# Kernel tuning notes

Hardware: AMD Instinct MI355X
Metric: run time of the kernel (lower is better)

## Reference

```python
import jax, jax.numpy as jnp
import numpy as np

B, S, D = 2, 2048, 1024
H = 16
HD = D // H  # 64

def setup_inputs() -> dict:
    key = jax.random.key(0)
    ks = jax.random.split(key, 5)
    scale = 0.02
    x = jax.random.normal(ks[0], (B, S, D), dtype=jnp.float32)
    w_attn = jax.random.normal(ks[1], (D, 3 * D), dtype=jnp.float32) * scale
    b_attn = jnp.zeros((3 * D,), dtype=jnp.float32)
    w_proj = jax.random.normal(ks[2], (D, D), dtype=jnp.float32) * scale
    b_proj = jnp.zeros((D,), dtype=jnp.float32)
    return {"x": x, "w_attn": w_attn, "b_attn": b_attn, "w_proj": w_proj, "b_proj": b_proj}

def reference(x, w_attn, b_attn, w_proj, b_proj):
    b, s, d = x.shape
    qkv = x @ w_attn + b_attn                      # [B,S,3D]
    q, k, v = jnp.split(qkv, 3, axis=-1)
    # [B,H,S,HD]
    q = q.reshape(b, s, H, HD).transpose(0, 2, 1, 3)
    k = k.reshape(b, s, H, HD).transpose(0, 2, 1, 3)
    v = v.reshape(b, s, H, HD).transpose(0, 2, 1, 3)
    scores = jnp.einsum('bhqd,bhkd->bhqk', q, k) * (1.0 / np.sqrt(HD))
    causal = jnp.tril(jnp.ones((s, s), dtype=bool))
    scores = jnp.where(causal[None, None], scores, -jnp.inf)
    attn = jax.nn.softmax(scores, axis=-1)
    out = jnp.einsum('bhqk,bhkd->bhqd', attn, v)   # [B,H,S,HD]
    out = out.transpose(0, 2, 1, 3).reshape(b, s, d)
    return out @ w_proj + b_proj
```

## Files before the change

kernel.cpp:

```cpp
#include <hip/hip_runtime.h>

#define B_  2
#define S_  2048
#define D_  1024
#define H_  16
#define HD_ 64
#define TD_ 3072
#define M_  (B_*S_)
#define NWORK_ 24

using bf16x8 = __attribute__((ext_vector_type(8))) short;
using bf16x4 = __attribute__((ext_vector_type(4))) short;
using f32x4  = __attribute__((ext_vector_type(4))) float;

typedef __attribute__((address_space(1))) unsigned int uint_g;
typedef __attribute__((address_space(3))) unsigned int uint_l;

#define MFMA32 __builtin_amdgcn_mfma_f32_16x16x32_bf16

#if defined(__has_builtin)
#if __has_builtin(__builtin_amdgcn_mfma_f32_16x16x16_bf16_1k)
#define MFMA16(a,b,c) __builtin_amdgcn_mfma_f32_16x16x16_bf16_1k(a,b,c,0,0,0)
#define HAVE_MFMA16 1
#elif __has_builtin(__builtin_amdgcn_mfma_f32_16x16x16bf16_1k)
#define MFMA16(a,b,c) __builtin_amdgcn_mfma_f32_16x16x16bf16_1k(a,b,c,0,0,0)
#define HAVE_MFMA16 1
#endif
#endif
#ifndef HAVE_MFMA16
static __device__ __forceinline__ f32x4 MFMA16_stub(bf16x4 a, bf16x4 b, f32x4 c) { return c; }
#define MFMA16(a,b,c) MFMA16_stub(a,b,c)
#endif

static __device__ __forceinline__ short f2bf(float f) {
    unsigned u = __float_as_uint(f);
    u += 0x7FFFu + ((u >> 16) & 1u);
    return (short)(u >> 16);
}
static __device__ __forceinline__ unsigned pack2bf(float a, float b) {
    return (unsigned)(unsigned short)f2bf(a) | ((unsigned)(unsigned short)f2bf(b) << 16);
}
static __device__ __forceinline__ void gload_lds16(const short* g, short* l) {
    __builtin_amdgcn_global_load_lds((const uint_g*)g, (uint_l*)l, 16, 0, 0);
}
static __device__ __forceinline__ void unpack8(uint4 u, float* f) {
    unsigned a0 = u.x, a1 = u.y, a2 = u.z, a3 = u.w;
    f[0] = __uint_as_float(a0 << 16); f[1] = __uint_as_float(a0 & 0xFFFF0000u);
    f[2] = __uint_as_float(a1 << 16); f[3] = __uint_as_float(a1 & 0xFFFF0000u);
    f[4] = __uint_as_float(a2 << 16); f[5] = __uint_as_float(a2 & 0xFFFF0000u);
    f[6] = __uint_as_float(a3 << 16); f[7] = __uint_as_float(a3 & 0xFFFF0000u);
}

__global__ void cast_x_kernel(const float* __restrict__ x, short* __restrict__ xb, int n4) {
    int i = blockIdx.x * blockDim.x + threadIdx.x;
    if (i >= n4) return;
    float4 v = *((const float4*)x + i);
    short4 o;
    o.x = f2bf(v.x); o.y = f2bf(v.y); o.z = f2bf(v.z); o.w = f2bf(v.w);
    *((short4*)xb + i) = o;
}

__global__ __launch_bounds__(256)
void wtrans_kernel(const float* __restrict__ W, short* __restrict__ Wt, int K, int N) {
    __shared__ float T[32][33];
    int n0 = blockIdx.x * 32, k0 = blockIdx.y * 32;
    int tx = threadIdx.x & 31, ty = threadIdx.x >> 5;
    #pragma unroll
    for (int i = 0; i < 4; ++i)
        T[ty + i * 8][tx] = W[(size_t)(k0 + ty + i * 8) * N + n0 + tx];
    __syncthreads();
    #pragma unroll
    for (int i = 0; i < 4; ++i)
        Wt[(size_t)(n0 + ty + i * 8) * K + k0 + tx] = f2bf(T[tx][ty + i * 8]);
}

__global__ __launch_bounds__(256)
void vtrans_kernel(const short* __restrict__ V, short* __restrict__ Vt) {
    __shared__ short T[32][33];
    int p  = blockIdx.z;
    int s0 = blockIdx.x * 32;
    int d0 = blockIdx.y * 32;
    int tx = threadIdx.x & 31, ty = threadIdx.x >> 5;
    const short* Vp  = V  + (size_t)p * S_ * HD_;
    short*       Vtp = Vt + (size_t)p * HD_ * S_;
    #pragma unroll
    for (int i = 0; i < 4; ++i)
        T[ty + i * 8][tx] = Vp[(s0 + ty + i * 8) * HD_ + d0 + tx];
    __syncthreads();
    #pragma unroll
    for (int i = 0; i < 4; ++i)
        Vtp[(size_t)(d0 + ty + i * 8) * S_ + s0 + tx] = T[tx][ty + i * 8];
}

template<int MODE>
__global__ __launch_bounds__(256)
void gemm_mfma_kernel(const short* __restrict__ A, const short* __restrict__ Bt,
                      const float* __restrict__ bias, float* __restrict__ Cf,
                      short* __restrict__ Qo, short* __restrict__ Ko, short* __restrict__ Vo,
                      int M, int N, int K) {
    __shared__ __align__(16) short As[128 * 32];
    __shared__ __align__(16) short Bs[128 * 32];

    const int tid  = threadIdx.x;
    const int w    = tid >> 6, lane = tid & 63;
    const int quad = lane >> 4, l16 = lane & 15;
    const int wr = (w >> 1) * 64, wc = (w & 1) * 64;
    const int rowBase = blockIdx.y * 128, colBase = blockIdx.x * 128;

    f32x4 acc[4][4];
    const f32x4 zero = {0.f, 0.f, 0.f, 0.f};
    #pragma unroll
    for (int i = 0; i < 4; ++i)
        #pragma unroll
        for (int j = 0; j < 4; ++j) acc[i][j] = zero;

    const int srow = lane >> 2;
    const int scol = (lane & 3) * 8;

    for (int k0 = 0; k0 < K; k0 += 32) {
        __syncthreads();
        gload_lds16(A  + (size_t)(rowBase + w * 16 + srow)      * K + k0 + scol, &As[(w * 16) * 32]);
        gload_lds16(A  + (size_t)(rowBase + 64 + w * 16 + srow) * K + k0 + scol, &As[(64 + w * 16) * 32]);
        gload_lds16(Bt + (size_t)(colBase + w * 16 + srow)      * K + k0 + scol, &Bs[(w * 16) * 32]);
        gload_lds16(Bt + (size_t)(colBase + 64 + w * 16 + srow) * K + k0 + scol, &Bs[(64 + w * 16) * 32]);
        __syncthreads();

        bf16x8 af[4], bf[4];
        #pragma unroll
        for (int t = 0; t < 4; ++t) {
            af[t] = *(const bf16x8*)&As[(wr + t * 16 + l16) * 32 + quad * 8];
            bf[t] = *(const bf16x8*)&Bs[(wc + t * 16 + l16) * 32 + quad * 8];
        }
        #pragma unroll
        for (int i = 0; i < 4; ++i)
            #pragma unroll
            for (int j = 0; j < 4; ++j)
                acc[i][j] = MFMA32(af[i], bf[j], acc[i][j], 0, 0, 0);
    }

    if (MODE == 0) {
        #pragma unroll
        for (int i = 0; i < 4; ++i) {
            int row = rowBase + wr + i * 16 + quad * 4;
            #pragma unroll
            for (int j = 0; j < 4; ++j) {
                int col = colBase + wc + j * 16 + l16;
                float bv = bias[col];
                #pragma unroll
                for (int r = 0; r < 4; ++r)
                    Cf[(size_t)(row + r) * N + col] = acc[i][j][r] + bv;
            }
        }
    } else {
        #pragma unroll
        for (int j = 0; j < 4; ++j) {
            int col = colBase + wc + j * 16 + l16;
            int sel = col >> 10, cr = col & 1023;
            int h = cr >> 6, d = cr & 63;
            float bv  = bias[col];
            short* dst = (sel == 0) ? Qo : (sel == 1) ? Ko : Vo;
            float  scl = (sel == 0) ? 0.125f : 1.0f;
            #pragma unroll
            for (int i = 0; i < 4; ++i) {
                int row = rowBase + wr + i * 16 + quad * 4;
                #pragma unroll
                for (int r = 0; r < 4; ++r) {
                    int rw = row + r;
                    int bb = rw >> 11, s = rw & 2047;
                    dst[((size_t)(bb * H_ + h) * S_ + s) * HD_ + d] =
                        f2bf((acc[i][j][r] + bv) * scl);
                }
            }
        }
    }
}

__global__ __launch_bounds__(256, 3)
void flash_mfma_kernel(const short* __restrict__ Qg, const short* __restrict__ Kg,
                       const short* __restrict__ Vtg,
                       short* __restrict__ pO, float* __restrict__ pl) {
    __shared__ __align__(16) short Ks[64][72];
    __shared__ __align__(16) short Vs[64][72];

    const int plane_id = blockIdx.x;
    const int y = blockIdx.y;
    int qi, kc;
    if (y < 8) { qi = y; kc = 0; }
    else       { qi = 8 + ((y - 8) >> 1); kc = (y - 8) & 1; }
    int nkt = 2 * qi + 2 - kc * 16;
    if (nkt > 16) nkt = 16;
    const int kvOrigin = kc * 1024;

    const int tid  = threadIdx.x;
    const int w    = tid >> 6, lane = tid & 63;
    const int quad = lane >> 4, l16 = lane & 15;
    const int qBase = qi * 128;
    const size_t plane = (size_t)plane_id * S_ * HD_;

    const int sr0 = tid >> 3;
    const int sc0 = (tid & 7) * 8;

    const int qsubA = qBase + w * 32;
    const short* QrowA = Qg + plane + (size_t)(qsubA + l16) * HD_ + quad * 8;
    const bf16x8 qa0 = *(const bf16x8*)(QrowA);
    const bf16x8 qa1 = *(const bf16x8*)(QrowA + 32);
    const short* QrowB = QrowA + 16 * HD_;
    const bf16x8 qb0 = *(const bf16x8*)(QrowB);
    const bf16x8 qb1 = *(const bf16x8*)(QrowB + 32);

    f32x4 oA[4], oB[4];
    const f32x4 zero = {0.f, 0.f, 0.f, 0.f};
    #pragma unroll
    for (int i = 0; i < 4; ++i) { oA[i] = zero; oB[i] = zero; }
    float lA = 0.f, lB = 0.f;
    const int q_globA = qsubA + l16;
    const int q_globB = qsubA + 16 + l16;
    const int q_wave_max = qsubA + 31;

    uint4 ka0, ka1, va0, va1;
    ka0 = *(const uint4*)(Kg  + plane + (size_t)(kvOrigin + sr0)      * HD_ + sc0);
    ka1 = *(const uint4*)(Kg  + plane + (size_t)(kvOrigin + sr0 + 32) * HD_ + sc0);
    va0 = *(const uint4*)(Vtg + plane + (size_t)sr0        * S_ + kvOrigin + sc0);
    va1 = *(const uint4*)(Vtg + plane + (size_t)(sr0 + 32) * S_ + kvOrigin + sc0);

    for (int j = 0; j < nkt; ++j) {
        __syncthreads();
        *(uint4*)&Ks[sr0][sc0]      = ka0;
        *(uint4*)&Ks[sr0 + 32][sc0] = ka1;
        *(uint4*)&Vs[sr0][sc0]      = va0;
        *(uint4*)&Vs[sr0 + 32][sc0] = va1;
        __syncthreads();

        if (j + 1 < nkt) {
            const int kvB = kvOrigin + (j + 1) * 64;
            ka0 = *(const uint4*)(Kg  + plane + (size_t)(kvB + sr0)      * HD_ + sc0);
            ka1 = *(const uint4*)(Kg  + plane + (size_t)(kvB + sr0 + 32) * HD_ + sc0);
            va0 = *(const uint4*)(Vtg + plane + (size_t)sr0        * S_ + kvB + sc0);
            va1 = *(const uint4*)(Vtg + plane + (size_t)(sr0 + 32) * S_ + kvB + sc0);
        }

        const int kvBase = kvOrigin + j * 64;
        if (kvBase > q_wave_max) continue;

        f32x4 sA[4], sB[4];
        #pragma unroll
        for (int ct = 0; ct < 4; ++ct) {
            bf16x8 kf0 = *(const bf16x8*)&Ks[ct * 16 + l16][quad * 8];
            bf16x8 kf1 = *(const bf16x8*)&Ks[ct * 16 + l16][32 + quad * 8];
            f32x4 a = zero, b = zero;
            a = MFMA32(kf0, qa0, a, 0, 0, 0);
            a = MFMA32(kf1, qa1, a, 0, 0, 0);
            b = MFMA32(kf0, qb0, b, 0, 0, 0);
            b = MFMA32(kf1, qb1, b, 0, 0, 0);
            sA[ct] = a; sB[ct] = b;
        }

        if (kvBase + 63 > qsubA) {
            #pragma unroll
            for (int ct = 0; ct < 4; ++ct) {
                int kv = kvBase + ct * 16 + quad * 4;
                #pragma unroll
                for (int r = 0; r < 4; ++r)
                    if (kv + r > q_globA) sA[ct][r] = -3.0e38f;
            }
        }
        if (kvBase + 63 > qsubA + 16) {
            #pragma unroll
            for (int ct = 0; ct < 4; ++ct) {
                int kv = kvBase + ct * 16 + quad * 4;
                #pragma unroll
                for (int r = 0; r < 4; ++r)
                    if (kv + r > q_globB) sB[ct][r] = -3.0e38f;
            }
        }

        #pragma unroll
        for (int ct = 0; ct < 4; ++ct) {
            float pa0 = __expf(sA[ct][0]), pa1 = __expf(sA[ct][1]);
            float pa2 = __expf(sA[ct][2]), pa3 = __expf(sA[ct][3]);
            float pb0 = __expf(sB[ct][0]), pb1 = __expf(sB[ct][1]);
            float pb2 = __expf(sB[ct][2]), pb3 = __expf(sB[ct][3]);
            lA += (pa0 + pa1) + (pa2 + pa3);
            lB += (pb0 + pb1) + (pb2 + pb3);
            bf16x4 pA, pB;
            *(unsigned*)&pA       = pack2bf(pa0, pa1);
            *((unsigned*)&pA + 1) = pack2bf(pa2, pa3);
            *(unsigned*)&pB       = pack2bf(pb0, pb1);
            *((unsigned*)&pB + 1) = pack2bf(pb2, pb3);
            #pragma unroll
            for (int dt = 0; dt < 4; ++dt) {
                bf16x4 vfr = *(const bf16x4*)&Vs[dt * 16 + l16][ct * 16 + quad * 4];
                oA[dt] = MFMA16(vfr, pA, oA[dt]);
                oB[dt] = MFMA16(vfr, pB, oB[dt]);
            }
        }
    }

    lA += __shfl_xor(lA, 16); lA += __shfl_xor(lA, 32);
    lB += __shfl_xor(lB, 16); lB += __shfl_xor(lB, 32);
    const size_t lbase = ((size_t)plane_id * NWORK_ + y) * 128 + w * 32;
    if (quad == 0) {
        pl[lbase + l16]      = lA;
        pl[lbase + 16 + l16] = lB;
    }

    __syncthreads();
    short* Pw = (w < 2) ? &Ks[w * 32][0] : &Vs[(w - 2) * 32][0];
    #pragma unroll
    for (int dt = 0; dt < 4; ++dt) {
        uint2 ua, ub;
        ua.x = pack2bf(oA[dt][0], oA[dt][1]);
        ua.y = pack2bf(oA[dt][2], oA[dt][3]);
        ub.x = pack2bf(oB[dt][0], oB[dt][1]);
        ub.y = pack2bf(oB[dt][2], oB[dt][3]);
        *(uint2*)&Pw[l16 * 72 + dt * 16 + quad * 4]        = ua;
        *(uint2*)&Pw[(16 + l16) * 72 + dt * 16 + quad * 4] = ub;
    }
    __builtin_amdgcn_s_waitcnt(0xC07F);
    short* outBase = pO + (((size_t)plane_id * NWORK_ + y) * 128 + w * 32) * 64;
    #pragma unroll
    for (int pass = 0; pass < 4; ++pass) {
        int r  = pass * 8 + (lane >> 3);
        int cs = (lane & 7) * 8;
        uint4 vv = *(const uint4*)&Pw[r * 72 + cs];
        *(uint4*)(outBase + r * 64 + cs) = vv;
    }
}

__global__ __launch_bounds__(256)
void reduce_kernel(const short* __restrict__ pO, const float* __restrict__ pl,
                   short* __restrict__ atb) {
    const int plane_id = blockIdx.x, qi = blockIdx.y;
    const int h = plane_id & (H_ - 1), b = plane_id >> 4;
    const int tid = threadIdx.x;
    const int row = tid >> 1;
    const int cb  = (tid & 1) * 32;

    int t0, nch;
    if (qi < 8) { t0 = qi; nch = 1; }
    else        { t0 = 8 + 2 * (qi - 8); nch = 2; }

    const size_t pbase = (((size_t)plane_id * NWORK_ + t0) * 128 + row) * 64 + cb;
    float f[32], g[8];
    unpack8(*(const uint4*)(pO + pbase),      f);
    unpack8(*(const uint4*)(pO + pbase + 8),  f + 8);
    unpack8(*(const uint4*)(pO + pbase + 16), f + 16);
    unpack8(*(const uint4*)(pO + pbase + 24), f + 24);
    float l = pl[((size_t)plane_id * NWORK_ + t0) * 128 + row];
    if (nch == 2) {
        #pragma unroll
        for (int c = 0; c < 4; ++c) {
            unpack8(*(const uint4*)(pO + pbase + 8192 + c * 8), g);
            #pragma unroll
            for (int i = 0; i < 8; ++i) f[c * 8 + i] += g[i];
        }
        l += pl[((size_t)plane_id * NWORK_ + t0 + 1) * 128 + row];
    }
    const float inv = 1.0f / l;
    short* dst = atb + (size_t)(b * S_ + qi * 128 + row) * D_ + h * HD_ + cb;
    #pragma unroll
    for (int c = 0; c < 4; ++c) {
        uint2 o2;
        o2.x = pack2bf(f[c * 8 + 0] * inv, f[c * 8 + 1] * inv);
        o2.y = pack2bf(f[c * 8 + 2] * inv, f[c * 8 + 3] * inv);
        uint2 o3;
        o3.x = pack2bf(f[c * 8 + 4] * inv, f[c * 8 + 5] * inv);
        o3.y = pack2bf(f[c * 8 + 6] * inv, f[c * 8 + 7] * inv);
        uint4 ov; ov.x = o2.x; ov.y = o2.y; ov.z = o3.x; ov.w = o3.y;
        *(uint4*)(dst + c * 8) = ov;
    }
}

extern "C" void kernel_launch(void* const* d_in, const int* in_sizes, int n_in,
                              void* d_out, int out_size, void* d_ws, size_t ws_size,
                              hipStream_t stream) {
    const float* x      = (const float*)d_in[0];
    const float* w_attn = (const float*)d_in[1];
    const float* b_attn = (const float*)d_in[2];
    const float* w_proj = (const float*)d_in[3];
    const float* b_proj = (const float*)d_in[4];
    float* out = (float*)d_out;

    char* ws = (char*)d_ws;
    short* xb  = (short*)ws; ws += (size_t)M_ * D_ * 2;
    short* wat = (short*)ws; ws += (size_t)TD_ * D_ * 2;
    short* wpt = (short*)ws; ws += (size_t)D_ * D_ * 2;
    short* qg  = (short*)ws; ws += (size_t)M_ * D_ * 2;
    short* kg  = (short*)ws; ws += (size_t)M_ * D_ * 2;
    short* vg  = (short*)ws; ws += (size_t)M_ * D_ * 2;
    short* vtg = (short*)ws; ws += (size_t)M_ * D_ * 2;
    short* atb = (short*)ws; ws += (size_t)M_ * D_ * 2;

    short* pO = (short*)d_ws;
    float* pl = (float*)((char*)d_ws + (size_t)32 * NWORK_ * 128 * 64 * 2);

    cast_x_kernel<<<(M_ * D_ / 4 + 255) / 256, 256, 0, stream>>>(x, xb, M_ * D_ / 4);
    wtrans_kernel<<<dim3(TD_ / 32, D_ / 32), 256, 0, stream>>>(w_attn, wat, D_, TD_);
    wtrans_kernel<<<dim3(D_ / 32, D_ / 32), 256, 0, stream>>>(w_proj, wpt, D_, D_);

    gemm_mfma_kernel<1><<<dim3(TD_ / 128, M_ / 128), 256, 0, stream>>>(
        xb, wat, b_attn, nullptr, qg, kg, vg, M_, TD_, D_);

    vtrans_kernel<<<dim3(S_ / 32, HD_ / 32, B_ * H_), 256, 0, stream>>>(vg, vtg);

    flash_mfma_kernel<<<dim3(B_ * H_, NWORK_), 256, 0, stream>>>(qg, kg, vtg, pO, pl);

    reduce_kernel<<<dim3(B_ * H_, S_ / 128), 256, 0, stream>>>(pO, pl, atb);

    gemm_mfma_kernel<0><<<dim3(D_ / 128, M_ / 128), 256, 0, stream>>>(
        atb, wpt, b_proj, out, nullptr, nullptr, nullptr, M_, D_, D_);
}
```

Before: 200.5 us.

## Split flash work finer, fuse prep kernels, shrink output GEMM tile

```diff
diff --git a/kernel.cpp b/kernel.cpp
--- a/kernel.cpp
+++ b/kernel.cpp
@@ -7,7 +7,8 @@
 #define HD_ 64
 #define TD_ 3072
 #define M_  (B_*S_)
-#define NWORK_ 24
+#define NWORK_ 40
+#define PO_SPLIT_ 896
 
 using bf16x8 = __attribute__((ext_vector_type(8))) short;
 using bf16x4 = __attribute__((ext_vector_type(4))) short;
@@ -50,21 +51,37 @@
     f[4] = __uint_as_float(a2 << 16); f[5] = __uint_as_float(a2 & 0xFFFF0000u);
     f[6] = __uint_as_float(a3 << 16); f[7] = __uint_as_float(a3 & 0xFFFF0000u);
 }
-
-__global__ void cast_x_kernel(const float* __restrict__ x, short* __restrict__ xb, int n4) {
-    int i = blockIdx.x * blockDim.x + threadIdx.x;
-    if (i >= n4) return;
-    float4 v = *((const float4*)x + i);
-    short4 o;
-    o.x = f2bf(v.x); o.y = f2bf(v.y); o.z = f2bf(v.z); o.w = f2bf(v.w);
-    *((short4*)xb + i) = o;
+static __device__ __forceinline__ const short* pO_ptr_c(const short* A, const short* B, int item) {
+    return (item < PO_SPLIT_) ? A + (size_t)item * 8192 : B + (size_t)(item - PO_SPLIT_) * 8192;
+}
+static __device__ __forceinline__ short* pO_ptr(short* A, short* B, int item) {
+    return (item < PO_SPLIT_) ? A + (size_t)item * 8192 : B + (size_t)(item - PO_SPLIT_) * 8192;
 }
 
 __global__ __launch_bounds__(256)
-void wtrans_kernel(const float* __restrict__ W, short* __restrict__ Wt, int K, int N) {
+void prep_kernel(const float* __restrict__ x, short* __restrict__ xb,
+                 const float* __restrict__ w_attn, short* __restrict__ wat,
+                 const float* __restrict__ w_proj, short* __restrict__ wpt) {
     __shared__ float T[32][33];
-    int n0 = blockIdx.x * 32, k0 = blockIdx.y * 32;
-    int tx = threadIdx.x & 31, ty = threadIdx.x >> 5;
+    const int id  = blockIdx.x;
+    const int tid = threadIdx.x;
+    if (id < 4096) {
+        int i = id * 256 + tid;
+        float4 v = *((const float4*)x + i);
+        short4 o;
+        o.x = f2bf(v.x); o.y = f2bf(v.y); o.z = f2bf(v.z); o.w = f2bf(v.w);
+        *((short4*)xb + i) = o;
+        return;
+    }
+    const float* W; short* Wt; int K, N, n0, k0;
+    if (id < 7168) {
+        int i = id - 4096; W = w_attn; Wt = wat; K = D_; N = TD_;
+        n0 = (i % 96) * 32; k0 = (i / 96) * 32;
+    } else {
+        int i = id - 7168; W = w_proj; Wt = wpt; K = D_; N = D_;
+        n0 = (i & 31) * 32; k0 = (i >> 5) * 32;
+    }
+    int tx = tid & 31, ty = tid >> 5;
     #pragma unroll
     for (int i = 0; i < 4; ++i)
         T[ty + i * 8][tx] = W[(size_t)(k0 + ty + i * 8) * N + n0 + tx];
@@ -92,12 +109,10 @@
         Vtp[(size_t)(d0 + ty + i * 8) * S_ + s0 + tx] = T[tx][ty + i * 8];
 }
 
-template<int MODE>
 __global__ __launch_bounds__(256)
-void gemm_mfma_kernel(const short* __restrict__ A, const short* __restrict__ Bt,
-                      const float* __restrict__ bias, float* __restrict__ Cf,
-                      short* __restrict__ Qo, short* __restrict__ Ko, short* __restrict__ Vo,
-                      int M, int N, int K) {
+void qkv_gemm_kernel(const short* __restrict__ A, const short* __restrict__ Bt,
+                     const float* __restrict__ bias,
+                     short* __restrict__ Qo, short* __restrict__ Ko, short* __restrict__ Vo) {
     __shared__ __align__(16) short As[128 * 32];
     __shared__ __align__(16) short Bs[128 * 32];
 
@@ -106,6 +121,7 @@
     const int quad = lane >> 4, l16 = lane & 15;
     const int wr = (w >> 1) * 64, wc = (w & 1) * 64;
     const int rowBase = blockIdx.y * 128, colBase = blockIdx.x * 128;
+    const int K = D_;
 
     f32x4 acc[4][4];
     const f32x4 zero = {0.f, 0.f, 0.f, 0.f};
@@ -138,58 +154,46 @@
                 acc[i][j] = MFMA32(af[i], bf[j], acc[i][j], 0, 0, 0);
     }
 
-    if (MODE == 0) {
+    #pragma unroll
+    for (int j = 0; j < 4; ++j) {
+        int col = colBase + wc + j * 16 + l16;
+        int sel = col >> 10, cr = col & 1023;
+        int h = cr >> 6, d = cr & 63;
+        float bv  = bias[col];
+        short* dst = (sel == 0) ? Qo : (sel == 1) ? Ko : Vo;
+        float  scl = (sel == 0) ? 0.125f : 1.0f;
         #pragma unroll
         for (int i = 0; i < 4; ++i) {
             int row = rowBase + wr + i * 16 + quad * 4;
             #pragma unroll
-            for (int j = 0; j < 4; ++j) {
-                int col = colBase + wc + j * 16 + l16;
-                float bv = bias[col];
-                #pragma unroll
-                for (int r = 0; r < 4; ++r)
-                    Cf[(size_t)(row + r) * N + col] = acc[i][j][r] + bv;
+            for (int r = 0; r < 4; ++r) {
+                int rw = row + r;
+                int bb = rw >> 11, s = rw & 2047;
+                dst[((size_t)(bb * H_ + h) * S_ + s) * HD_ + d] =
+                    f2bf((acc[i][j][r] + bv) * scl);
             }
         }
-    } else {
-        #pragma unroll
-        for (int j = 0; j < 4; ++j) {
-            int col = colBase + wc + j * 16 + l16;
-            int sel = col >> 10, cr = col & 1023;
-            int h = cr >> 6, d = cr & 63;
-            float bv  = bias[col];
-            short* dst = (sel == 0) ? Qo : (sel == 1) ? Ko : Vo;
-            float  scl = (sel == 0) ? 0.125f : 1.0f;
-            #pragma unroll
-            for (int i = 0; i < 4; ++i) {
-                int row = rowBase + wr + i * 16 + quad * 4;
-                #pragma unroll
-                for (int r = 0; r < 4; ++r) {
-                    int rw = row + r;
-                    int bb = rw >> 11, s = rw & 2047;
-                    dst[((size_t)(bb * H_ + h) * S_ + s) * HD_ + d] =
-                        f2bf((acc[i][j][r] + bv) * scl);
-                }
-            }
-        }
-    }
-}
-
-__global__ __launch_bounds__(256, 3)
+    }
+}
+
+__global__ __launch_bounds__(256, 6)
 void flash_mfma_kernel(const short* __restrict__ Qg, const short* __restrict__ Kg,
                        const short* __restrict__ Vtg,
-                       short* __restrict__ pO, float* __restrict__ pl) {
+                       short* __restrict__ poA, short* __restrict__ poB,
+                       float* __restrict__ pl) {
     __shared__ __align__(16) short Ks[64][72];
     __shared__ __align__(16) short Vs[64][72];
 
     const int plane_id = blockIdx.x;
-    const int y = blockIdx.y;
-    int qi, kc;
-    if (y < 8) { qi = y; kc = 0; }
-    else       { qi = 8 + ((y - 8) >> 1); kc = (y - 8) & 1; }
-    int nkt = 2 * qi + 2 - kc * 16;
-    if (nkt > 16) nkt = 16;
-    const int kvOrigin = kc * 1024;
+    const int y = (int)(gridDim.y - 1) - (int)blockIdx.y;
+    const int g = (y < 4) ? 0 : (y < 12) ? 1 : (y < 24) ? 2 : 3;
+    const int rem = y - 2 * g * (g + 1);
+    const int qi = 4 * g + rem / (g + 1);
+    const int kc = rem - (rem / (g + 1)) * (g + 1);
+    int nkt = 2 * qi + 2 - kc * 8;
+    if (nkt > 8) nkt = 8;
+    const int kvOrigin = kc * 512;
+    const int item = plane_id * NWORK_ + y;
 
     const int tid  = threadIdx.x;
     const int w    = tid >> 6, lane = tid & 63;
@@ -298,7 +302,7 @@
 
     lA += __shfl_xor(lA, 16); lA += __shfl_xor(lA, 32);
     lB += __shfl_xor(lB, 16); lB += __shfl_xor(lB, 32);
-    const size_t lbase = ((size_t)plane_id * NWORK_ + y) * 128 + w * 32;
+    const size_t lbase = (size_t)item * 128 + w * 32;
     if (quad == 0) {
         pl[lbase + l16]      = lA;
         pl[lbase + 16 + l16] = lB;
@@ -317,7 +321,7 @@
         *(uint2*)&Pw[(16 + l16) * 72 + dt * 16 + quad * 4] = ub;
     }
     __builtin_amdgcn_s_waitcnt(0xC07F);
-    short* outBase = pO + (((size_t)plane_id * NWORK_ + y) * 128 + w * 32) * 64;
+    short* outBase = pO_ptr(poA, poB, item) + (size_t)(w * 32) * 64;
     #pragma unroll
     for (int pass = 0; pass < 4; ++pass) {
         int r  = pass * 8 + (lane >> 3);
@@ -328,46 +332,99 @@
 }
 
 __global__ __launch_bounds__(256)
-void reduce_kernel(const short* __restrict__ pO, const float* __restrict__ pl,
-                   short* __restrict__ atb) {
+void reduce_kernel(const short* __restrict__ poA, const short* __restrict__ poB,
+                   const float* __restrict__ pl, short* __restrict__ atb) {
     const int plane_id = blockIdx.x, qi = blockIdx.y;
     const int h = plane_id & (H_ - 1), b = plane_id >> 4;
     const int tid = threadIdx.x;
     const int row = tid >> 1;
     const int cb  = (tid & 1) * 32;
 
-    int t0, nch;
-    if (qi < 8) { t0 = qi; nch = 1; }
-    else        { t0 = 8 + 2 * (qi - 8); nch = 2; }
-
-    const size_t pbase = (((size_t)plane_id * NWORK_ + t0) * 128 + row) * 64 + cb;
-    float f[32], g[8];
-    unpack8(*(const uint4*)(pO + pbase),      f);
-    unpack8(*(const uint4*)(pO + pbase + 8),  f + 8);
-    unpack8(*(const uint4*)(pO + pbase + 16), f + 16);
-    unpack8(*(const uint4*)(pO + pbase + 24), f + 24);
-    float l = pl[((size_t)plane_id * NWORK_ + t0) * 128 + row];
-    if (nch == 2) {
+    const int g = qi >> 2;
+    const int t0 = 2 * g * (g + 1) + (qi - 4 * g) * (g + 1);
+    const int nch = g + 1;
+    const int item0 = plane_id * NWORK_ + t0;
+
+    float f[32];
+    #pragma unroll
+    for (int i = 0; i < 32; ++i) f[i] = 0.f;
+    float l = 0.f;
+    for (int ch = 0; ch < nch; ++ch) {
+        const short* p = pO_ptr_c(poA, poB, item0 + ch) + (size_t)row * 64 + cb;
+        float g8[8];
         #pragma unroll
         for (int c = 0; c < 4; ++c) {
-            unpack8(*(const uint4*)(pO + pbase + 8192 + c * 8), g);
-            #pragma unroll
-            for (int i = 0; i < 8; ++i) f[c * 8 + i] += g[i];
-        }
-        l += pl[((size_t)plane_id * NWORK_ + t0 + 1) * 128 + row];
+            unpack8(*(const uint4*)(p + c * 8), g8);
+            #pragma unroll
+            for (int i = 0; i < 8; ++i) f[c * 8 + i] += g8[i];
+        }
+        l += pl[(size_t)(item0 + ch) * 128 + row];
     }
     const float inv = 1.0f / l;
     short* dst = atb + (size_t)(b * S_ + qi * 128 + row) * D_ + h * HD_ + cb;
     #pragma unroll
     for (int c = 0; c < 4; ++c) {
-        uint2 o2;
-        o2.x = pack2bf(f[c * 8 + 0] * inv, f[c * 8 + 1] * inv);
-        o2.y = pack2bf(f[c * 8 + 2] * inv, f[c * 8 + 3] * inv);
-        uint2 o3;
-        o3.x = pack2bf(f[c * 8 + 4] * inv, f[c * 8 + 5] * inv);
-        o3.y = pack2bf(f[c * 8 + 6] * inv, f[c * 8 + 7] * inv);
-        uint4 ov; ov.x = o2.x; ov.y = o2.y; ov.z = o3.x; ov.w = o3.y;
+        uint4 ov;
+        ov.x = pack2bf(f[c * 8 + 0] * inv, f[c * 8 + 1] * inv);
+        ov.y = pack2bf(f[c * 8 + 2] * inv, f[c * 8 + 3] * inv);
+        ov.z = pack2bf(f[c * 8 + 4] * inv, f[c * 8 + 5] * inv);
+        ov.w = pack2bf(f[c * 8 + 6] * inv, f[c * 8 + 7] * inv);
         *(uint4*)(dst + c * 8) = ov;
+    }
+}
+
+__global__ __launch_bounds__(256)
+void gemm2_mfma_kernel(const short* __restrict__ A, const short* __restrict__ Bt,
+                       const float* __restrict__ bias, float* __restrict__ Cf) {
+    __shared__ __align__(16) short As[64 * 32];
+    __shared__ __align__(16) short Bs[128 * 32];
+
+    const int tid  = threadIdx.x;
+    const int w    = tid >> 6, lane = tid & 63;
+    const int quad = lane >> 4, l16 = lane & 15;
+    const int rowBase = blockIdx.y * 64, colBase = blockIdx.x * 128;
+    const int K = D_;
+
+    f32x4 acc[4][2];
+    const f32x4 zero = {0.f, 0.f, 0.f, 0.f};
+    #pragma unroll
+    for (int i = 0; i < 4; ++i) { acc[i][0] = zero; acc[i][1] = zero; }
+
+    const int srow = lane >> 2;
+    const int scol = (lane & 3) * 8;
+
+    for (int k0 = 0; k0 < K; k0 += 32) {
+        __syncthreads();
+        gload_lds16(A  + (size_t)(rowBase + w * 16 + srow)      * K + k0 + scol, &As[(w * 16) * 32]);
+        gload_lds16(Bt + (size_t)(colBase + w * 16 + srow)      * K + k0 + scol, &Bs[(w * 16) * 32]);
+        gload_lds16(Bt + (size_t)(colBase + 64 + w * 16 + srow) * K + k0 + scol, &Bs[(64 + w * 16) * 32]);
+        __syncthreads();
+
+        bf16x8 af[4], bf[2];
+        #pragma unroll
+        for (int t = 0; t < 4; ++t)
+            af[t] = *(const bf16x8*)&As[(t * 16 + l16) * 32 + quad * 8];
+        #pragma unroll
+        for (int t = 0; t < 2; ++t)
+            bf[t] = *(const bf16x8*)&Bs[(w * 32 + t * 16 + l16) * 32 + quad * 8];
+        #pragma unroll
+        for (int i = 0; i < 4; ++i)
+            #pragma unroll
+            for (int j = 0; j < 2; ++j)
+                acc[i][j] = MFMA32(af[i], bf[j], acc[i][j], 0, 0, 0);
+    }
+
+    #pragma unroll
+    for (int i = 0; i < 4; ++i) {
+        int row = rowBase + i * 16 + quad * 4;
+        #pragma unroll
+        for (int j = 0; j < 2; ++j) {
+            int col = colBase + w * 32 + j * 16 + l16;
+            float bv = bias[col];
+            #pragma unroll
+            for (int r = 0; r < 4; ++r)
+                Cf[(size_t)(row + r) * D_ + col] = acc[i][j][r] + bv;
+        }
     }
 }
 
@@ -382,31 +439,31 @@
     float* out = (float*)d_out;
 
     char* ws = (char*)d_ws;
+    short* wpt = (short*)ws; ws += (size_t)D_ * D_ * 2;
     short* xb  = (short*)ws; ws += (size_t)M_ * D_ * 2;
     short* wat = (short*)ws; ws += (size_t)TD_ * D_ * 2;
-    short* wpt = (short*)ws; ws += (size_t)D_ * D_ * 2;
     short* qg  = (short*)ws; ws += (size_t)M_ * D_ * 2;
     short* kg  = (short*)ws; ws += (size_t)M_ * D_ * 2;
-    short* vg  = (short*)ws; ws += (size_t)M_ * D_ * 2;
     short* vtg = (short*)ws; ws += (size_t)M_ * D_ * 2;
     short* atb = (short*)ws; ws += (size_t)M_ * D_ * 2;
-
-    short* pO = (short*)d_ws;
-    float* pl = (float*)((char*)d_ws + (size_t)32 * NWORK_ * 128 * 64 * 2);
-
-    cast_x_kernel<<<(M_ * D_ / 4 + 255) / 256, 256, 0, stream>>>(x, xb, M_ * D_ / 4);
-    wtrans_kernel<<<dim3(TD_ / 32, D_ / 32), 256, 0, stream>>>(w_attn, wat, D_, TD_);
-    wtrans_kernel<<<dim3(D_ / 32, D_ / 32), 256, 0, stream>>>(w_proj, wpt, D_, D_);
-
-    gemm_mfma_kernel<1><<<dim3(TD_ / 128, M_ / 128), 256, 0, stream>>>(
-        xb, wat, b_attn, nullptr, qg, kg, vg, M_, TD_, D_);
+    short* vg  = (short*)ws; ws += (size_t)M_ * D_ * 2;
+
+    short* poA = xb;
+    short* poB = vg;
+    float* pl  = (float*)ws;
+
+    prep_kernel<<<8192, 256, 0, stream>>>(x, xb, w_attn, wat, w_proj, wpt);
+
+    qkv_gemm_kernel<<<dim3(TD_ / 128, M_ / 128), 256, 0, stream>>>(
+        xb, wat, b_attn, qg, kg, vg);
 
     vtrans_kernel<<<dim3(S_ / 32, HD_ / 32, B_ * H_), 256, 0, stream>>>(vg, vtg);
 
-    flash_mfma_kernel<<<dim3(B_ * H_, NWORK_), 256, 0, stream>>>(qg, kg, vtg, pO, pl);
-
-    reduce_kernel<<<dim3(B_ * H_, S_ / 128), 256, 0, stream>>>(pO, pl, atb);
-
-    gemm_mfma_kernel<0><<<dim3(D_ / 128, M_ / 128), 256, 0, stream>>>(
-        atb, wpt, b_proj, out, nullptr, nullptr, nullptr, M_, D_, D_);
-}
+    flash_mfma_kernel<<<dim3(B_ * H_, NWORK_), 256, 0, stream>>>(
+        qg, kg, vtg, poA, poB, pl);
+
+    reduce_kernel<<<dim3(B_ * H_, S_ / 128), 256, 0, stream>>>(poA, poB, pl, atb);
+
+    gemm2_mfma_kernel<<<dim3(D_ / 128, M_ / 64), 256, 0, stream>>>(
+        atb, wpt, b_proj, out);
+}
```

Measured after the change: 319.9 us. 1.6x slower.
